# Performance work log

Hardware: AMD Instinct MI355X
Metric: run time of the kernel (lower is better)

## Reference

```python
import jax, jax.numpy as jnp
import numpy as np

ROUTINGS = 3

def squash(x):
    # x: [..., O]; squash along last dim
    norm = jnp.linalg.norm(x, axis=-1, keepdims=True)
    scale = norm ** 2 / (1 + norm ** 2) / (norm + 1e-9)
    return scale * x

def setup_inputs() -> dict:
    key = jax.random.key(0)
    k1, k2 = jax.random.split(key)
    B, K, I, O, C = 256, 10, 1152, 16, 8
    x = jax.random.normal(k1, (B, I, C), dtype=jnp.float32)
    w = jax.random.normal(k2, (K, I, O, C), dtype=jnp.float32) * 0.05
    return {"x": x, "w": w}

def reference(x, w):
    # x: [B, I, Cin], w: [K, I, O, Cin]
    # u_hat[b,k,i,o] = sum_c w[k,i,o,c] * x[b,i,c]
    u_hat = jnp.einsum('kioc,bic->bkio', w, x)  # [B, K, I, O]
    B, K, I, O = u_hat.shape
    b = jnp.zeros((B, K, I, 1), dtype=u_hat.dtype)
    # routing iterations (fixed small loop); intermediate iters use detached u_hat
    u_hat_d = jax.lax.stop_gradient(u_hat)
    for _ in range(ROUTINGS - 1):
        c = jax.nn.softmax(b, axis=1)              # softmax over output capsules K
        s = jnp.sum(c * u_hat_d, axis=2)           # [B, K, O]
        v = squash(s)                              # [B, K, O]
        uv = jnp.einsum('bkio,bko->bki', u_hat_d, v)[..., None]  # [B, K, I, 1]
        b = b + uv
    c = jax.nn.softmax(b, axis=1)
    s = jnp.sum(c * u_hat, axis=2)
    v = squash(s)
    return v  # [B, K, O]
```

## Files before the change

kernel.cpp:

```cpp
#include <hip/hip_runtime.h>

#define B_ 256
#define K_ 10
#define I_ 1152
#define O_ 16
#define C_ 8
#define BKO (B_*K_*O_)
#define NX 72

static __device__ __forceinline__ unsigned short f32_bf16(float f) {
    unsigned int u = __float_as_uint(f);
    u += 0x7FFFu + ((u >> 16) & 1u);
    return (unsigned short)(u >> 16);
}

template <int CTRL>
static __device__ __forceinline__ float dpp_add(float v) {
    int x = __builtin_amdgcn_update_dpp(0, __float_as_int(v), CTRL, 0xF, 0xF, true);
    return v + __int_as_float(x);
}
static __device__ __forceinline__ float row16_sum(float v) {
    v = dpp_add<0xB1>(v);
    v = dpp_add<0x4E>(v);
    v = dpp_add<0x141>(v);
    v = dpp_add<0x140>(v);
    return v;
}

__global__ __launch_bounds__(256) void uhat_kernel(
    const float* __restrict__ x, const float* __restrict__ w,
    unsigned short* __restrict__ u, float* __restrict__ part)
{
    __shared__ float w_lds[16 * 132];
    __shared__ float p_lds[2][64 * 17];
    const int t   = threadIdx.x;
    const int i_l = t & 15, tg = t >> 4;
    const int i0  = blockIdx.x * 16;
    const int b0  = blockIdx.y * 64 + tg * 4;
    const int kb  = blockIdx.z * 2;
    const int i   = i0 + i_l;
    const bool row_leader = (i_l == 0);

    float4 xr[4][2];
#pragma unroll
    for (int bb = 0; bb < 4; bb++) {
        const float4* xp = (const float4*)(x + ((size_t)(b0 + bb) * I_ + i) * C_);
        xr[bb][0] = xp[0];
        xr[bb][1] = xp[1];
    }

#pragma unroll
    for (int kk = 0; kk < 2; kk++) {
        const int k = kb + kk;
        __syncthreads();
        const float4* ws = (const float4*)(w + ((size_t)k * I_ + i0) * O_ * C_);
#pragma unroll
        for (int r = 0; r < 2; r++) {
            int idx = r * 256 + t;
            int ii = idx >> 5, rem = idx & 31;
            *(float4*)&w_lds[ii * 132 + rem * 4] = ws[idx];
        }
        __syncthreads();

        unsigned int pk[4][8];
#pragma unroll
        for (int oo = 0; oo < 8; oo++) {
            float d[4][2];
#pragma unroll
            for (int h = 0; h < 2; h++) {
                const int o = oo * 2 + h;
                const float4 w0 = *(const float4*)&w_lds[i_l * 132 + o * 8];
                const float4 w1 = *(const float4*)&w_lds[i_l * 132 + o * 8 + 4];
#pragma unroll
                for (int bb = 0; bb < 4; bb++) {
                    d[bb][h] = w0.x*xr[bb][0].x + w0.y*xr[bb][0].y
                             + w0.z*xr[bb][0].z + w0.w*xr[bb][0].w
                             + w1.x*xr[bb][1].x + w1.y*xr[bb][1].y
                             + w1.z*xr[bb][1].z + w1.w*xr[bb][1].w;
                }
            }
#pragma unroll
            for (int bb = 0; bb < 4; bb++) {
#pragma unroll
                for (int h = 0; h < 2; h++) {
                    const float rs = row16_sum(d[bb][h]);
                    if (row_leader)
                        p_lds[kk][(tg * 4 + bb) * 17 + oo * 2 + h] = rs;
                }
            }
#pragma unroll
            for (int bb = 0; bb < 4; bb++)
                pk[bb][oo] = (unsigned int)f32_bf16(d[bb][0]) |
                             ((unsigned int)f32_bf16(d[bb][1]) << 16);
        }
#pragma unroll
        for (int bb = 0; bb < 4; bb++) {
            unsigned int* dst = (unsigned int*)
                (u + (((size_t)(b0 + bb) * K_ + k) * I_ + i) * O_);
            *(uint4*)(dst)     = make_uint4(pk[bb][0], pk[bb][1], pk[bb][2], pk[bb][3]);
            *(uint4*)(dst + 4) = make_uint4(pk[bb][4], pk[bb][5], pk[bb][6], pk[bb][7]);
        }
    }

    __syncthreads();
    {
        const int bl = t >> 2, o4 = (t & 3) * 4;
#pragma unroll
        for (int kk = 0; kk < 2; kk++) {
            float4 v;
            v.x = p_lds[kk][bl * 17 + o4 + 0];
            v.y = p_lds[kk][bl * 17 + o4 + 1];
            v.z = p_lds[kk][bl * 17 + o4 + 2];
            v.w = p_lds[kk][bl * 17 + o4 + 3];
            *(float4*)&part[(((size_t)blockIdx.x * K_ + kb + kk) * 256
                             + blockIdx.y * 64 + bl) * O_ + o4] = v;
        }
    }
}

static __device__ __forceinline__ void sweep(
    const unsigned short* __restrict__ ub, int i_l,
    const float* __restrict__ v_lds, int og, float acc[K_][2])
{
#pragma unroll
    for (int k = 0; k < K_; k++) { acc[k][0] = 0.f; acc[k][1] = 0.f; }

    unsigned int P[K_], Q[K_];
#pragma unroll
    for (int k = 0; k < K_; k++)
        P[k] = *(const unsigned int*)(ub + ((size_t)k * I_ + i_l) * O_);

#pragma unroll 1
    for (int ic = 0; ic < 9; ic++) {
        if (ic + 1 < 9) {
            const int i = (ic + 1) * 128 + i_l;
#pragma unroll
            for (int k = 0; k < K_; k++)
                Q[k] = *(const unsigned int*)(ub + ((size_t)k * I_ + i) * O_);
        }
        float c[K_];
        float Z = 0.f;
#pragma unroll
        for (int k = 0; k < K_; k++) {
            const float f0 = __uint_as_float(P[k] << 16);
            const float f1 = __uint_as_float(P[k] & 0xffff0000u);
            float lk = f0 * v_lds[k * 16 + og * 2]
                     + f1 * v_lds[k * 16 + og * 2 + 1];
            lk += __shfl_xor(lk, 1);
            lk += __shfl_xor(lk, 2);
            lk += __shfl_xor(lk, 4);
            c[k] = __expf(lk);
            Z += c[k];
        }
        const float inv = 1.0f / Z;
#pragma unroll
        for (int k = 0; k < K_; k++) {
            const float ck = c[k] * inv;
            const float f0 = __uint_as_float(P[k] << 16);
            const float f1 = __uint_as_float(P[k] & 0xffff0000u);
            acc[k][0] = fmaf(ck, f0, acc[k][0]);
            acc[k][1] = fmaf(ck, f1, acc[k][1]);
        }
#pragma unroll
        for (int k = 0; k < K_; k++) P[k] = Q[k];
    }
}

static __device__ __forceinline__ void block_reduce(
    float acc[K_][2], float* __restrict__ red, int lane, int wv)
{
#pragma unroll
    for (int k = 0; k < K_; k++)
#pragma unroll
        for (int j = 0; j < 2; j++) {
            float a = acc[k][j];
            a += __shfl_xor(a, 8); a += __shfl_xor(a, 16); a += __shfl_xor(a, 32);
            acc[k][j] = a;
        }
    if (lane < 8) {
#pragma unroll
        for (int k = 0; k < K_; k++)
            *(float2*)&red[wv * 160 + k * 16 + lane * 2] =
                make_float2(acc[k][0], acc[k][1]);
    }
    __syncthreads();
}

static __device__ __forceinline__ float sum16(const float* __restrict__ red, int t)
{
    float s = 0.f;
#pragma unroll
    for (int wgi = 0; wgi < 16; wgi++) s += red[wgi * 160 + t];
    return s;
}

static __device__ __forceinline__ float squash_v(float s) {
    float n2 = s * s;
    n2 += __shfl_xor(n2, 1); n2 += __shfl_xor(n2, 2);
    n2 += __shfl_xor(n2, 4); n2 += __shfl_xor(n2, 8);
    const float norm = sqrtf(n2);
    return s * (n2 / (1.0f + n2) / (norm + 1e-9f));
}

__global__ __launch_bounds__(1024) void route_all(
    const unsigned short* __restrict__ u, const float* __restrict__ part,
    float* __restrict__ out)
{
    __shared__ float red[16 * 160];
    __shared__ float v_lds[160];
    __shared__ float v1_lds[160];

    const int t    = threadIdx.x;
    const int og   = t & 7, i_l = t >> 3;
    const int b    = blockIdx.x;
    const int lane = t & 63, wv = t >> 6;

    const unsigned short* ub = u + (size_t)b * K_ * I_ * O_ + og * 2;
    float acc[K_][2];

    if (t < 160) {
        const int k = t >> 4, o = t & 15;
        const float* pb = part + ((size_t)k * 256 + b) * O_ + o;
        float s = 0.f;
#pragma unroll
        for (int xb = 0; xb < NX; xb++)
            s += pb[(size_t)xb * BKO];
        float v = squash_v(s * (1.0f / K_));
        v1_lds[t] = v;
        v_lds[t]  = v;
    }
    __syncthreads();

    sweep(ub, i_l, v_lds, og, acc);
    block_reduce(acc, red, lane, wv);
    float v12 = 0.f;
    if (t < 160) v12 = v1_lds[t] + squash_v(sum16(red, t));
    __syncthreads();
    if (t < 160) v_lds[t] = v12;
    __syncthreads();

    sweep(ub, i_l, v_lds, og, acc);
    block_reduce(acc, red, lane, wv);
    if (t < 160)
        out[(size_t)b * 160 + t] = squash_v(sum16(red, t));
}

extern "C" void kernel_launch(void* const* d_in, const int* in_sizes, int n_in,
                              void* d_out, int out_size, void* d_ws, size_t ws_size,
                              hipStream_t stream)
{
    const float* x = (const float*)d_in[0];
    const float* w = (const float*)d_in[1];
    float* outp = (float*)d_out;

    float* part = (float*)d_ws;
    unsigned short* u = (unsigned short*)(part + (size_t)NX * BKO);

    uhat_kernel<<<dim3(72, 4, 5), 256, 0, stream>>>(x, w, u, part);
    route_all<<<B_, 1024, 0, stream>>>(u, part, outp);
}
```

Baseline: 133.8 us.

## Split uhat grid per capsule and widen routing threads to four outputs

The u_hat kernel now handles one output capsule per block instead of two, doubling the grid to 2880 blocks for more parallelism at the cost of reloading x per capsule. The routing kernel halves its block to 512 threads, with each thread loading a uint2 (four bf16 values) and keeping four accumulators per capsule. This cuts the shuffle depth for the logit reduction and the number of partial sums in the block reduction. It also raises register pressure and halves the in-flight threads per routing block.

```diff
diff --git a/kernel.cpp b/kernel.cpp
--- a/kernel.cpp
+++ b/kernel.cpp
@@ -32,12 +32,12 @@
     unsigned short* __restrict__ u, float* __restrict__ part)
 {
     __shared__ float w_lds[16 * 132];
-    __shared__ float p_lds[2][64 * 17];
+    __shared__ float p_lds[64 * 17];
     const int t   = threadIdx.x;
     const int i_l = t & 15, tg = t >> 4;
     const int i0  = blockIdx.x * 16;
     const int b0  = blockIdx.y * 64 + tg * 4;
-    const int kb  = blockIdx.z * 2;
+    const int k   = blockIdx.z;
     const int i   = i0 + i_l;
     const bool row_leader = (i_l == 0);
 
@@ -49,10 +49,7 @@
         xr[bb][1] = xp[1];
     }
 
-#pragma unroll
-    for (int kk = 0; kk < 2; kk++) {
-        const int k = kb + kk;
-        __syncthreads();
+    {
         const float4* ws = (const float4*)(w + ((size_t)k * I_ + i0) * O_ * C_);
 #pragma unroll
         for (int r = 0; r < 2; r++) {
@@ -60,75 +57,74 @@
             int ii = idx >> 5, rem = idx & 31;
             *(float4*)&w_lds[ii * 132 + rem * 4] = ws[idx];
         }
-        __syncthreads();
-
-        unsigned int pk[4][8];
-#pragma unroll
-        for (int oo = 0; oo < 8; oo++) {
-            float d[4][2];
+    }
+    __syncthreads();
+
+    unsigned int pk[4][8];
+#pragma unroll
+    for (int oo = 0; oo < 8; oo++) {
+        float d[4][2];
+#pragma unroll
+        for (int h = 0; h < 2; h++) {
+            const int o = oo * 2 + h;
+            const float4 w0 = *(const float4*)&w_lds[i_l * 132 + o * 8];
+            const float4 w1 = *(const float4*)&w_lds[i_l * 132 + o * 8 + 4];
+#pragma unroll
+            for (int bb = 0; bb < 4; bb++) {
+                d[bb][h] = w0.x*xr[bb][0].x + w0.y*xr[bb][0].y
+                         + w0.z*xr[bb][0].z + w0.w*xr[bb][0].w
+                         + w1.x*xr[bb][1].x + w1.y*xr[bb][1].y
+                         + w1.z*xr[bb][1].z + w1.w*xr[bb][1].w;
+            }
+        }
+#pragma unroll
+        for (int bb = 0; bb < 4; bb++) {
 #pragma unroll
             for (int h = 0; h < 2; h++) {
-                const int o = oo * 2 + h;
-                const float4 w0 = *(const float4*)&w_lds[i_l * 132 + o * 8];
-                const float4 w1 = *(const float4*)&w_lds[i_l * 132 + o * 8 + 4];
-#pragma unroll
-                for (int bb = 0; bb < 4; bb++) {
-                    d[bb][h] = w0.x*xr[bb][0].x + w0.y*xr[bb][0].y
-                             + w0.z*xr[bb][0].z + w0.w*xr[bb][0].w
-                             + w1.x*xr[bb][1].x + w1.y*xr[bb][1].y
-                             + w1.z*xr[bb][1].z + w1.w*xr[bb][1].w;
-                }
+                const float rs = row16_sum(d[bb][h]);
+                if (row_leader)
+                    p_lds[(tg * 4 + bb) * 17 + oo * 2 + h] = rs;
             }
-#pragma unroll
-            for (int bb = 0; bb < 4; bb++) {
-#pragma unroll
-                for (int h = 0; h < 2; h++) {
-                    const float rs = row16_sum(d[bb][h]);
-                    if (row_leader)
-                        p_lds[kk][(tg * 4 + bb) * 17 + oo * 2 + h] = rs;
-                }
-            }
-#pragma unroll
-            for (int bb = 0; bb < 4; bb++)
-                pk[bb][oo] = (unsigned int)f32_bf16(d[bb][0]) |
-                             ((unsigned int)f32_bf16(d[bb][1]) << 16);
-        }
-#pragma unroll
-        for (int bb = 0; bb < 4; bb++) {
-            unsigned int* dst = (unsigned int*)
-                (u + (((size_t)(b0 + bb) * K_ + k) * I_ + i) * O_);
-            *(uint4*)(dst)     = make_uint4(pk[bb][0], pk[bb][1], pk[bb][2], pk[bb][3]);
-            *(uint4*)(dst + 4) = make_uint4(pk[bb][4], pk[bb][5], pk[bb][6], pk[bb][7]);
-        }
+        }
+#pragma unroll
+        for (int bb = 0; bb < 4; bb++)
+            pk[bb][oo] = (unsigned int)f32_bf16(d[bb][0]) |
+                         ((unsigned int)f32_bf16(d[bb][1]) << 16);
+    }
+#pragma unroll
+    for (int bb = 0; bb < 4; bb++) {
+        unsigned int* dst = (unsigned int*)
+            (u + (((size_t)(b0 + bb) * K_ + k) * I_ + i) * O_);
+        *(uint4*)(dst)     = make_uint4(pk[bb][0], pk[bb][1], pk[bb][2], pk[bb][3]);
+        *(uint4*)(dst + 4) = make_uint4(pk[bb][4], pk[bb][5], pk[bb][6], pk[bb][7]);
     }
 
     __syncthreads();
     {
         const int bl = t >> 2, o4 = (t & 3) * 4;
-#pragma unroll
-        for (int kk = 0; kk < 2; kk++) {
-            float4 v;
-            v.x = p_lds[kk][bl * 17 + o4 + 0];
-            v.y = p_lds[kk][bl * 17 + o4 + 1];
-            v.z = p_lds[kk][bl * 17 + o4 + 2];
-            v.w = p_lds[kk][bl * 17 + o4 + 3];
-            *(float4*)&part[(((size_t)blockIdx.x * K_ + kb + kk) * 256
-                             + blockIdx.y * 64 + bl) * O_ + o4] = v;
-        }
+        float4 v;
+        v.x = p_lds[bl * 17 + o4 + 0];
+        v.y = p_lds[bl * 17 + o4 + 1];
+        v.z = p_lds[bl * 17 + o4 + 2];
+        v.w = p_lds[bl * 17 + o4 + 3];
+        *(float4*)&part[(((size_t)blockIdx.x * K_ + k) * 256
+                         + blockIdx.y * 64 + bl) * O_ + o4] = v;
     }
 }
 
 static __device__ __forceinline__ void sweep(
     const unsigned short* __restrict__ ub, int i_l,
-    const float* __restrict__ v_lds, int og, float acc[K_][2])
-{
-#pragma unroll
-    for (int k = 0; k < K_; k++) { acc[k][0] = 0.f; acc[k][1] = 0.f; }
-
-    unsigned int P[K_], Q[K_];
+    const float* __restrict__ v_lds, int og, float acc[K_][4])
+{
 #pragma unroll
     for (int k = 0; k < K_; k++)
-        P[k] = *(const unsigned int*)(ub + ((size_t)k * I_ + i_l) * O_);
+#pragma unroll
+        for (int j = 0; j < 4; j++) acc[k][j] = 0.f;
+
+    uint2 P[K_], Q[K_];
+#pragma unroll
+    for (int k = 0; k < K_; k++)
+        P[k] = *(const uint2*)(ub + ((size_t)k * I_ + i_l) * O_);
 
 #pragma unroll 1
     for (int ic = 0; ic < 9; ic++) {
@@ -136,19 +132,20 @@
             const int i = (ic + 1) * 128 + i_l;
 #pragma unroll
             for (int k = 0; k < K_; k++)
-                Q[k] = *(const unsigned int*)(ub + ((size_t)k * I_ + i) * O_);
+                Q[k] = *(const uint2*)(ub + ((size_t)k * I_ + i) * O_);
         }
         float c[K_];
         float Z = 0.f;
 #pragma unroll
         for (int k = 0; k < K_; k++) {
-            const float f0 = __uint_as_float(P[k] << 16);
-            const float f1 = __uint_as_float(P[k] & 0xffff0000u);
-            float lk = f0 * v_lds[k * 16 + og * 2]
-                     + f1 * v_lds[k * 16 + og * 2 + 1];
+            const float f0 = __uint_as_float(P[k].x << 16);
+            const float f1 = __uint_as_float(P[k].x & 0xffff0000u);
+            const float f2 = __uint_as_float(P[k].y << 16);
+            const float f3 = __uint_as_float(P[k].y & 0xffff0000u);
+            const float* vk = &v_lds[k * 16 + og * 4];
+            float lk = f0 * vk[0] + f1 * vk[1] + f2 * vk[2] + f3 * vk[3];
             lk += __shfl_xor(lk, 1);
             lk += __shfl_xor(lk, 2);
-            lk += __shfl_xor(lk, 4);
             c[k] = __expf(lk);
             Z += c[k];
         }
@@ -156,10 +153,10 @@
 #pragma unroll
         for (int k = 0; k < K_; k++) {
             const float ck = c[k] * inv;
-            const float f0 = __uint_as_float(P[k] << 16);
-            const float f1 = __uint_as_float(P[k] & 0xffff0000u);
-            acc[k][0] = fmaf(ck, f0, acc[k][0]);
-            acc[k][1] = fmaf(ck, f1, acc[k][1]);
+            acc[k][0] = fmaf(ck, __uint_as_float(P[k].x << 16),        acc[k][0]);
+            acc[k][1] = fmaf(ck, __uint_as_float(P[k].x & 0xffff0000u), acc[k][1]);
+            acc[k][2] = fmaf(ck, __uint_as_float(P[k].y << 16),        acc[k][2]);
+            acc[k][3] = fmaf(ck, __uint_as_float(P[k].y & 0xffff0000u), acc[k][3]);
         }
 #pragma unroll
         for (int k = 0; k < K_; k++) P[k] = Q[k];
@@ -167,30 +164,31 @@
 }
 
 static __device__ __forceinline__ void block_reduce(
-    float acc[K_][2], float* __restrict__ red, int lane, int wv)
+    float acc[K_][4], float* __restrict__ red, int lane, int wv)
 {
 #pragma unroll
     for (int k = 0; k < K_; k++)
 #pragma unroll
-        for (int j = 0; j < 2; j++) {
+        for (int j = 0; j < 4; j++) {
             float a = acc[k][j];
-            a += __shfl_xor(a, 8); a += __shfl_xor(a, 16); a += __shfl_xor(a, 32);
+            a += __shfl_xor(a, 4);  a += __shfl_xor(a, 8);
+            a += __shfl_xor(a, 16); a += __shfl_xor(a, 32);
             acc[k][j] = a;
         }
-    if (lane < 8) {
+    if (lane < 4) {
 #pragma unroll
         for (int k = 0; k < K_; k++)
-            *(float2*)&red[wv * 160 + k * 16 + lane * 2] =
-                make_float2(acc[k][0], acc[k][1]);
-    }
-    __syncthreads();
-}
-
-static __device__ __forceinline__ float sum16(const float* __restrict__ red, int t)
+            *(float4*)&red[wv * 160 + k * 16 + lane * 4] =
+                make_float4(acc[k][0], acc[k][1], acc[k][2], acc[k][3]);
+    }
+    __syncthreads();
+}
+
+static __device__ __forceinline__ float sum8(const float* __restrict__ red, int t)
 {
     float s = 0.f;
 #pragma unroll
-    for (int wgi = 0; wgi < 16; wgi++) s += red[wgi * 160 + t];
+    for (int wgi = 0; wgi < 8; wgi++) s += red[wgi * 160 + t];
     return s;
 }
 
@@ -202,21 +200,21 @@
     return s * (n2 / (1.0f + n2) / (norm + 1e-9f));
 }
 
-__global__ __launch_bounds__(1024) void route_all(
+__global__ __launch_bounds__(512) void route_all(
     const unsigned short* __restrict__ u, const float* __restrict__ part,
     float* __restrict__ out)
 {
-    __shared__ float red[16 * 160];
+    __shared__ float red[8 * 160];
     __shared__ float v_lds[160];
     __shared__ float v1_lds[160];
 
     const int t    = threadIdx.x;
-    const int og   = t & 7, i_l = t >> 3;
+    const int og   = t & 3, i_l = t >> 2;
     const int b    = blockIdx.x;
     const int lane = t & 63, wv = t >> 6;
 
-    const unsigned short* ub = u + (size_t)b * K_ * I_ * O_ + og * 2;
-    float acc[K_][2];
+    const unsigned short* ub = u + (size_t)b * K_ * I_ * O_ + og * 4;
+    float acc[K_][4];
 
     if (t < 160) {
         const int k = t >> 4, o = t & 15;
@@ -234,7 +232,7 @@
     sweep(ub, i_l, v_lds, og, acc);
     block_reduce(acc, red, lane, wv);
     float v12 = 0.f;
-    if (t < 160) v12 = v1_lds[t] + squash_v(sum16(red, t));
+    if (t < 160) v12 = v1_lds[t] + squash_v(sum8(red, t));
     __syncthreads();
     if (t < 160) v_lds[t] = v12;
     __syncthreads();
@@ -242,7 +240,7 @@
     sweep(ub, i_l, v_lds, og, acc);
     block_reduce(acc, red, lane, wv);
     if (t < 160)
-        out[(size_t)b * 160 + t] = squash_v(sum16(red, t));
+        out[(size_t)b * 160 + t] = squash_v(sum8(red, t));
 }
 
 extern "C" void kernel_launch(void* const* d_in, const int* in_sizes, int n_in,
@@ -256,6 +254,6 @@
     float* part = (float*)d_ws;
     unsigned short* u = (unsigned short*)(part + (size_t)NX * BKO);
 
-    uhat_kernel<<<dim3(72, 4, 5), 256, 0, stream>>>(x, w, u, part);
-    route_all<<<B_, 1024, 0, stream>>>(u, part, outp);
-}
+    uhat_kernel<<<dim3(72, 4, 10), 256, 0, stream>>>(x, w, u, part);
+    route_all<<<B_, 512, 0, stream>>>(u, part, outp);
+}
```

New measurement: 126.3 us. -5.6%, faster.
